# Optimization experiments

Measured on AMD Instinct MI355X. Metric: run time of the kernel, lower is better.

The kernel has to match this reference:

```python
import jax, jax.numpy as jnp
import numpy as np

N = 100000   # nodes
E = 1600000  # edges (before self loops)
F = 64       # num_features
H = 64       # hidden_channels
C = 10       # num_classes
G = 128      # graphs in batch
NEG_SLOPE = 0.2


def setup_inputs() -> dict:
    key = jax.random.key(0)
    ks = jax.random.split(key, 16)
    x = jax.random.normal(ks[0], (N, F), dtype=jnp.float32)
    edge_index = jax.random.randint(ks[1], (2, E), 0, N, dtype=jnp.int64)
    batch = jnp.sort(jax.random.randint(ks[2], (N,), 0, G, dtype=jnp.int64))
    def glorot(k, shape):
        fan = shape[0] + shape[-1]
        return jax.random.uniform(k, shape, jnp.float32, -1.0, 1.0) * np.sqrt(6.0 / fan)
    return {
        "x": x, "edge_index": edge_index, "batch": batch,
        # GATConv 1 (F -> H)
        "W1": glorot(ks[3], (F, H)), "as1": glorot(ks[4], (H,)), "ad1": glorot(ks[5], (H,)), "b1": jnp.zeros((H,), jnp.float32),
        # GATConv 2 (H -> H)
        "W2": glorot(ks[6], (H, H)), "as2": glorot(ks[7], (H,)), "ad2": glorot(ks[8], (H,)), "b2": jnp.zeros((H,), jnp.float32),
        # MLP head
        "mw1": glorot(ks[9], (H, H)), "mb1": jnp.zeros((H,), jnp.float32),
        "mw2": glorot(ks[10], (H, C)), "mb2": jnp.zeros((C,), jnp.float32),
    }


def gat_conv(x, src, dst, W, a_s, a_d, b):
    # x: [N, Fin] -> h: [N, Fout]
    h = x @ W
    # per-node attention halves, gathered per edge (heads=1)
    al_s = h @ a_s   # [N]
    al_d = h @ a_d   # [N]
    e = jax.nn.leaky_relu(al_s[src] + al_d[dst], NEG_SLOPE)  # [E']
    # segment softmax over incoming edges of each destination node
    m = jax.ops.segment_max(e, dst, num_segments=N)
    ex = jnp.exp(e - m[dst])
    denom = jax.ops.segment_sum(ex, dst, num_segments=N)
    alpha = ex / denom[dst]                                   # [E']
    # weighted scatter-add of source features
    out = jax.ops.segment_sum(alpha[:, None] * h[src], dst, num_segments=N)
    return out + b


def reference(x, edge_index, batch, W1, as1, ad1, b1, W2, as2, ad2, b2, mw1, mb1, mw2, mb2):
    # add self loops (PyG GATConv default)
    loop = jnp.arange(N, dtype=edge_index.dtype)
    src = jnp.concatenate([edge_index[0], loop])
    dst = jnp.concatenate([edge_index[1], loop])

    h = gat_conv(x, src, dst, W1, as1, ad1, b1)
    h = jax.nn.elu(h)  # dropout p=0.5 is identity in eval mode
    h = gat_conv(h, src, dst, W2, as2, ad2, b2)
    h = jax.nn.elu(h)

    h = jax.nn.relu(h @ mw1 + mb1) @ mw2 + mb2   # MLP [N, C]
    return jax.ops.segment_sum(h, batch, num_segments=G)  # global_add_pool [G, C]
```

## Files before the change

kernel.cpp:

```cpp
#include <hip/hip_runtime.h>
#include <hip/hip_bf16.h>
#include <math.h>

#define SHIFT 20.0f
#define T_PER 8
#define TILE (256 * T_PER)
#define BCAP 5248
#define LS_T 1024

typedef __bf16 bf16x8 __attribute__((ext_vector_type(8)));
typedef float  f32x4  __attribute__((ext_vector_type(4)));

__device__ __forceinline__ unsigned f2bf(float f) {
    unsigned u = __float_as_uint(f);
    return (u + 0x7fffu + ((u >> 16) & 1u)) >> 16;
}

__global__ void setup_kernel(int* __restrict__ bcur, int K2,
                             float* __restrict__ Pz, int nPz,
                             const float* __restrict__ W1,
                             const float* __restrict__ as1, const float* __restrict__ ad1,
                             const float* __restrict__ W2,
                             const float* __restrict__ as2, const float* __restrict__ ad2,
                             const float* __restrict__ mw1,
                             uint4* __restrict__ Wf1, uint4* __restrict__ Wf2,
                             uint4* __restrict__ mwf)
{
    int t = threadIdx.x;
    if (blockIdx.x == 0) {
        for (int i = t; i < K2; i += 256) bcur[i * 16] = i * BCAP;
        for (int i = t; i < nPz; i += 256) Pz[i] = 0.f;
        return;
    }
    __shared__ float wasad[256];
    {
        int k = t & 63;
        const float* W  = (t < 128) ? W1 : W2;
        const float* av = (t < 64) ? as1 : (t < 128) ? ad1 : (t < 192) ? as2 : ad2;
        float s = 0.f;
        for (int n = 0; n < 64; n++) s = fmaf(W[k * 64 + n], av[n], s);
        wasad[t] = s;
    }
    __syncthreads();

    for (int idx = t; idx < 1792; idx += 256) {
        const float* W; const float* wv; uint4* dst; int rem;
        if (idx < 640)       { rem = idx;        W = W1;  wv = &wasad[0];   dst = Wf1; }
        else if (idx < 1280) { rem = idx - 640;  W = W2;  wv = &wasad[128]; dst = Wf2; }
        else                 { rem = idx - 1280; W = mw1; wv = nullptr;     dst = mwf; }
        int pair = rem >> 6, l = rem & 63;
        int tt = pair >> 1, s = pair & 1;
        int kb = s * 32 + (l >> 4) * 8;
        unsigned d[4];
        if (tt < 4) {
            int n = tt * 16 + (l & 15);
            #pragma unroll
            for (int j = 0; j < 4; j++)
                d[j] = f2bf(W[(kb + 2 * j) * 64 + n]) |
                       (f2bf(W[(kb + 2 * j + 1) * 64 + n]) << 16);
        } else {
            int n0 = l & 15;
            #pragma unroll
            for (int j = 0; j < 4; j++) {
                float v0 = (n0 == 0) ? wv[kb + 2 * j]     : (n0 == 1) ? wv[64 + kb + 2 * j]     : 0.f;
                float v1 = (n0 == 0) ? wv[kb + 2 * j + 1] : (n0 == 1) ? wv[64 + kb + 2 * j + 1] : 0.f;
                d[j] = f2bf(v0) | (f2bf(v1) << 16);
            }
        }
        dst[pair * 64 + l] = make_uint4(d[0], d[1], d[2], d[3]);
    }
}

__device__ __forceinline__ void multisplit_body(
    unsigned char* lds, const int* __restrict__ esrc, const int* __restrict__ edst,
    int* __restrict__ bcur, unsigned* __restrict__ pairbuf,
    int nE, int tot, int K2, int tile)
{
    int* lhist = (int*)lds;
    int* lbase = lhist + 512;
    int t = threadIdx.x;
    int base = tile * TILE;
    for (int i = t; i < K2; i += 256) lhist[i] = 0;
    __syncthreads();

    unsigned pk[T_PER];
    int loc[T_PER];
    #pragma unroll
    for (int i = 0; i < T_PER; i++) {
        int e = base + t + i * 256;
        if (e < tot) {
            int s = (e < nE) ? esrc[e] : (e - nE);
            int d = (e < nE) ? edst[e] : (e - nE);
            int b = d >> 8;
            pk[i] = ((unsigned)s << 8) | (unsigned)(d & 255);
            int idx = atomicAdd(&lhist[b], 1);
            loc[i] = (b << 20) | idx;
        } else loc[i] = -1;
    }
    __syncthreads();
    for (int i = t; i < K2; i += 256) {
        int c = lhist[i];
        lbase[i] = (c > 0) ? atomicAdd(&bcur[i * 16], c) : 0;
    }
    __syncthreads();
    #pragma unroll
    for (int i = 0; i < T_PER; i++) {
        if (loc[i] >= 0)
            pairbuf[lbase[loc[i] >> 20] + (loc[i] & 0xFFFFF)] = pk[i];
    }
}

__device__ __forceinline__ void gemm_body(
    unsigned char* lds, const void* __restrict__ Xv, int x_is_bf16,
    const uint4* __restrict__ Wf, __hip_bfloat16* __restrict__ Hout,
    float* __restrict__ als, float* __restrict__ ald, int nN, int b0)
{
    int t = threadIdx.x, lane = t & 63, wv = t >> 6;

    uint4 wf[10];
    #pragma unroll
    for (int p = 0; p < 10; p++) wf[p] = Wf[p * 64 + lane];

    if (x_is_bf16) {
        const uint4* X4 = (const uint4*)Xv;
        int limit = nN * 8;
        #pragma unroll
        for (int k = 0; k < 8; k++) {
            int dst = t + k * 256;
            int idx = b0 * 8 + dst;
            if (idx < limit) {
                int r = dst >> 3, c = dst & 7;
                *(uint4*)(lds + r * 144 + c * 16) = X4[idx];
            }
        }
    } else {
        const float4* Xf = (const float4*)Xv;
        int limit = nN * 16;
        #pragma unroll
        for (int k = 0; k < 16; k++) {
            int dst = t + k * 256;
            int idx = b0 * 16 + dst;
            if (idx < limit) {
                float4 v = Xf[idx];
                uint2 r2;
                r2.x = f2bf(v.x) | (f2bf(v.y) << 16);
                r2.y = f2bf(v.z) | (f2bf(v.w) << 16);
                int r = dst >> 4, c = dst & 15;
                *(uint2*)(lds + r * 144 + c * 8) = r2;
            }
        }
    }
    __syncthreads();

    f32x4 acc[4][5] = {};
    int rbase = wv * 64;
    #pragma unroll
    for (int s = 0; s < 2; s++) {
        #pragma unroll
        for (int rf = 0; rf < 4; rf++) {
            const uint4 av = *(const uint4*)(lds + (rbase + rf * 16 + (lane & 15)) * 144
                                                 + s * 64 + (lane >> 4) * 16);
            bf16x8 a = __builtin_bit_cast(bf16x8, av);
            #pragma unroll
            for (int tt = 0; tt < 5; tt++) {
                bf16x8 b = __builtin_bit_cast(bf16x8, wf[tt * 2 + s]);
                acc[rf][tt] = __builtin_amdgcn_mfma_f32_16x16x32_bf16(a, b, acc[rf][tt], 0, 0, 0);
            }
        }
    }

    int q = lane >> 4, c = lane & 15;
    #pragma unroll
    for (int rf = 0; rf < 4; rf++) {
        #pragma unroll
        for (int r = 0; r < 4; r++) {
            int n = b0 + rbase + rf * 16 + q * 4 + r;
            if (n < nN) {
                #pragma unroll
                for (int tt = 0; tt < 4; tt++)
                    Hout[(size_t)n * 64 + tt * 16 + c] = __float2bfloat16(acc[rf][tt][r]);
                if (c == 0)      als[n] = acc[rf][4][r];
                else if (c == 1) ald[n] = acc[rf][4][r];
            }
        }
    }
}

__global__ __launch_bounds__(256) void ms_gemm_kernel(
    const int* __restrict__ esrc, const int* __restrict__ edst,
    int* __restrict__ bcur, unsigned* __restrict__ pairbuf,
    int nE, int nN, int K2, int nTiles,
    const void* __restrict__ Xv, const uint4* __restrict__ Wf,
    __hip_bfloat16* __restrict__ Hout,
    float* __restrict__ als, float* __restrict__ ald)
{
    __shared__ __align__(16) unsigned char lds[256 * 144];
    if (blockIdx.x < nTiles) {
        multisplit_body(lds, esrc, edst, bcur, pairbuf, nE, nE + nN, K2, blockIdx.x);
    } else {
        gemm_body(lds, Xv, 0, Wf, Hout, als, ald, nN, (blockIdx.x - nTiles) * 256);
    }
}

__global__ __launch_bounds__(256) void gemm_att_mfma(
    const void* __restrict__ Xv, int x_is_bf16,
    const uint4* __restrict__ Wf,
    __hip_bfloat16* __restrict__ Hout,
    float* __restrict__ als, float* __restrict__ ald, int nN)
{
    __shared__ __align__(16) unsigned char lds[256 * 144];
    gemm_body(lds, Xv, x_is_bf16, Wf, Hout, als, ald, nN, blockIdx.x * 256);
}

__global__ __launch_bounds__(LS_T) void local_scatter_kernel(
    const unsigned* __restrict__ pairbuf, const int* __restrict__ bcur,
    int2* __restrict__ rp2, int* __restrict__ csr_src, int nN, int K2)
{
    __shared__ unsigned seg[BCAP];
    __shared__ int lh[256];
    __shared__ int cur[256];
    __shared__ int psum[256];
    int b = blockIdx.x;
    int t = threadIdx.x;
    int d0 = b * 256;
    int nd = min(256, nN - d0);
    int lo = b * BCAP;
    int hi = bcur[b * 16];
    int len = min(hi - lo, BCAP);

    if (t < 256) lh[t] = 0;
    for (int j = t; j < len; j += LS_T) seg[j] = pairbuf[lo + j];
    __syncthreads();
    for (int j = t; j < len; j += LS_T) atomicAdd(&lh[seg[j] & 255u], 1);
    __syncthreads();

    int v = (t < 256) ? lh[t] : 0;
    if (t < 256) psum[t] = v;
    __syncthreads();
    for (int off = 1; off < 256; off <<= 1) {
        int u = (t < 256 && t >= off) ? psum[t - off] : 0;
        __syncthreads();
        if (t < 256) psum[t] += u;
        __syncthreads();
    }
    if (t < 256) {
        int e0 = lo + psum[t] - v;
        cur[t] = e0;
        if (t < nd) rp2[d0 + t] = make_int2(e0, v);
    }
    __syncthreads();

    for (int j = t; j < len; j += LS_T) {
        unsigned w = seg[j];
        int pos = atomicAdd(&cur[w & 255u], 1);
        csr_src[pos] = (int)(w >> 8);
    }
}

__global__ __launch_bounds__(256) void pull_kernel(
    const int* __restrict__ csr_src, const int2* __restrict__ rp2,
    const unsigned* __restrict__ Hu,
    const float* __restrict__ als, const float* __restrict__ ald,
    const float* __restrict__ bias,
    __hip_bfloat162* __restrict__ out2, int nN)
{
    int lane = threadIdx.x & 63;
    int half = lane >> 5;
    int fl = lane & 31;
    int wid  = (blockIdx.x * blockDim.x + threadIdx.x) >> 6;
    int nw   = (gridDim.x * blockDim.x) >> 6;
    float2 bl2 = ((const float2*)bias)[fl];

    for (int d = wid; d < nN; d += nw) {
        int2 rp = rp2[d];
        int s0 = rp.x, m = rp.y;
        float aldd = ald[d];
        float aclo = 0.f, achi = 0.f, den = 0.f;

        for (int base = 0; base < m; base += 64) {
            int j = base + lane;
            bool v = (j < m);
            int sl = v ? csr_src[s0 + j] : 0;
            float ex = 0.f;
            if (v) {
                float sc = als[sl] + aldd;
                sc = (sc > 0.f) ? sc : 0.2f * sc;
                ex = __expf(sc - SHIFT);
            }
            float es = ex;
            #pragma unroll
            for (int off = 32; off > 0; off >>= 1) es += __shfl_xor(es, off);
            den += es;

            int mm = min(64, m - base);
            int sA = __shfl(sl, half), sB = __shfl(sl, 2 + half);
            float eA = __shfl(ex, half), eB = __shfl(ex, 2 + half);
            unsigned dA = Hu[((unsigned)sA << 5) | fl];
            unsigned dB = Hu[((unsigned)sB << 5) | fl];
            for (int i2 = 0; i2 < mm; i2 += 4) {
                int i4 = (i2 + 4) & 63;
                int   sA2 = __shfl(sl, i4 + half);
                int   sB2 = __shfl(sl, i4 + 2 + half);
                float eA2 = __shfl(ex, i4 + half);
                float eB2 = __shfl(ex, i4 + 2 + half);
                unsigned dA2 = Hu[((unsigned)sA2 << 5) | fl];
                unsigned dB2 = Hu[((unsigned)sB2 << 5) | fl];
                aclo = fmaf(eA, __uint_as_float(dA << 16), aclo);
                achi = fmaf(eA, __uint_as_float(dA & 0xffff0000u), achi);
                aclo = fmaf(eB, __uint_as_float(dB << 16), aclo);
                achi = fmaf(eB, __uint_as_float(dB & 0xffff0000u), achi);
                sA = sA2; sB = sB2; eA = eA2; eB = eB2; dA = dA2; dB = dB2;
            }
        }
        aclo += __shfl_xor(aclo, 32);
        achi += __shfl_xor(achi, 32);
        float v0 = aclo / den + bl2.x;
        float v1 = achi / den + bl2.y;
        v0 = (v0 > 0.f) ? v0 : expm1f(v0);
        v1 = (v1 > 0.f) ? v1 : expm1f(v1);
        if (half == 0) {
            __hip_bfloat162 pk;
            pk.x = __float2bfloat16(v0);
            pk.y = __float2bfloat16(v1);
            out2[((unsigned)d << 5) | fl] = pk;
        }
    }
}

__global__ __launch_bounds__(256) void mlp_pool_mfma(
    const uint4* __restrict__ Hin,
    const uint4* __restrict__ mwf, const float* __restrict__ mb1,
    const int* __restrict__ batch,
    float* __restrict__ P, float* __restrict__ Pcnt, int nN)
{
    __shared__ __align__(16) unsigned char lds[256 * 144];
    int t = threadIdx.x, lane = t & 63, wv = t >> 6;
    int b0 = blockIdx.x * 256;

    uint4 wf[8];
    #pragma unroll
    for (int p = 0; p < 8; p++) wf[p] = mwf[p * 64 + lane];

    int limit = nN * 8;
    #pragma unroll
    for (int k = 0; k < 8; k++) {
        int dst = t + k * 256;
        int idx = b0 * 8 + dst;
        if (idx < limit) {
            int r = dst >> 3, c = dst & 7;
            *(uint4*)(lds + r * 144 + c * 16) = Hin[idx];
        }
    }
    __syncthreads();

    f32x4 acc[4][4] = {};
    int rbase = wv * 64;
    #pragma unroll
    for (int s = 0; s < 2; s++) {
        #pragma unroll
        for (int rf = 0; rf < 4; rf++) {
            const uint4 av = *(const uint4*)(lds + (rbase + rf * 16 + (lane & 15)) * 144
                                                 + s * 64 + (lane >> 4) * 16);
            bf16x8 a = __builtin_bit_cast(bf16x8, av);
            #pragma unroll
            for (int tt = 0; tt < 4; tt++) {
                bf16x8 b = __builtin_bit_cast(bf16x8, wf[tt * 2 + s]);
                acc[rf][tt] = __builtin_amdgcn_mfma_f32_16x16x32_bf16(a, b, acc[rf][tt], 0, 0, 0);
            }
        }
    }

    int q = lane >> 4, c = lane & 15;
    float bl0 = mb1[c], bl1 = mb1[16 + c], bl2 = mb1[32 + c], bl3 = mb1[48 + c];
    float r0 = 0.f, r1 = 0.f, r2 = 0.f, r3 = 0.f, ccnt = 0.f;
    int gcur = -1;
    #pragma unroll
    for (int rf = 0; rf < 4; rf++) {
        #pragma unroll
        for (int r = 0; r < 4; r++) {
            int n = b0 + rbase + rf * 16 + q * 4 + r;
            if (n < nN) {
                int g = batch[n];
                if (g != gcur) {
                    if (gcur >= 0) {
                        atomicAdd(&P[(size_t)gcur * 64 + c],      r0);
                        atomicAdd(&P[(size_t)gcur * 64 + 16 + c], r1);
                        atomicAdd(&P[(size_t)gcur * 64 + 32 + c], r2);
                        atomicAdd(&P[(size_t)gcur * 64 + 48 + c], r3);
                        if (c == 0) atomicAdd(&Pcnt[gcur], ccnt);
                    }
                    gcur = g; r0 = r1 = r2 = r3 = 0.f; ccnt = 0.f;
                }
                r0 += fmaxf(acc[rf][0][r] + bl0, 0.f);
                r1 += fmaxf(acc[rf][1][r] + bl1, 0.f);
                r2 += fmaxf(acc[rf][2][r] + bl2, 0.f);
                r3 += fmaxf(acc[rf][3][r] + bl3, 0.f);
                ccnt += 1.f;
            }
        }
    }
    if (gcur >= 0) {
        atomicAdd(&P[(size_t)gcur * 64 + c],      r0);
        atomicAdd(&P[(size_t)gcur * 64 + 16 + c], r1);
        atomicAdd(&P[(size_t)gcur * 64 + 32 + c], r2);
        atomicAdd(&P[(size_t)gcur * 64 + 48 + c], r3);
        if (c == 0) atomicAdd(&Pcnt[gcur], ccnt);
    }
}

__global__ void head_out_kernel(const float* __restrict__ P,
                                const float* __restrict__ Pcnt,
                                const float* __restrict__ mw2,
                                const float* __restrict__ mb2,
                                float* __restrict__ out, int nOut)
{
    int t = blockIdx.x * blockDim.x + threadIdx.x;
    if (t >= nOut) return;
    int g = t / 10, j = t % 10;
    float s = mb2[j] * Pcnt[g];
    const float* pr = P + (size_t)g * 64;
    #pragma unroll
    for (int k = 0; k < 64; k++) s = fmaf(pr[k], mw2[k * 10 + j], s);
    out[t] = s;
}

extern "C" void kernel_launch(void* const* d_in, const int* in_sizes, int n_in,
                              void* d_out, int out_size, void* d_ws, size_t ws_size,
                              hipStream_t stream)
{
    const float* x   = (const float*)d_in[0];
    const int*  eidx = (const int*)d_in[1];
    const int* batch = (const int*)d_in[2];
    const float* W1  = (const float*)d_in[3];
    const float* as1 = (const float*)d_in[4];
    const float* ad1 = (const float*)d_in[5];
    const float* b1  = (const float*)d_in[6];
    const float* W2  = (const float*)d_in[7];
    const float* as2 = (const float*)d_in[8];
    const float* ad2 = (const float*)d_in[9];
    const float* b2  = (const float*)d_in[10];
    const float* mw1 = (const float*)d_in[11];
    const float* mb1 = (const float*)d_in[12];
    const float* mw2 = (const float*)d_in[13];
    const float* mb2 = (const float*)d_in[14];
    float* out = (float*)d_out;

    int nN = in_sizes[0] / 64;
    int nE = in_sizes[1] / 2;
    int tot = nE + nN;
    int K2 = (nN + 255) >> 8;
    int G  = out_size / 10;
    const int* esrc = eidx;
    const int* edst = eidx + nE;

    float* ws = (float*)d_ws;
    size_t NF = (size_t)nN * 64;
    size_t capTot = (size_t)K2 * BCAP;
    float* bufA   = ws;
    float* bufB   = ws + NF;
    float* als    = ws + 2 * NF;
    float* ald    = als + nN;
    int2* rp2     = (int2*)(ald + nN);
    int* csr_src  = (int*)(rp2 + nN);
    int* bcur     = csr_src + capTot;
    float* P      = (float*)(bcur + K2 * 16 + 15);
    float* Pcnt   = P + (size_t)G * 64;
    uintptr_t wb  = ((uintptr_t)(Pcnt + G) + 255) & ~(uintptr_t)255;
    uint4* Wf1    = (uint4*)wb;
    uint4* Wf2    = Wf1 + 640;
    uint4* mwf    = Wf2 + 640;
    unsigned* pairbuf = (unsigned*)bufA;
    __hip_bfloat16* hbf = (__hip_bfloat16*)bufB;

    dim3 blk(256);
    int nTiles = (tot + TILE - 1) / TILE;
    int nT256 = (nN + 255) / 256;

    setup_kernel<<<2, blk, 0, stream>>>(bcur, K2, P, G * 64 + G,
                                        W1, as1, ad1, W2, as2, ad2, mw1,
                                        Wf1, Wf2, mwf);
    ms_gemm_kernel<<<nTiles + nT256, blk, 0, stream>>>(
        esrc, edst, bcur, pairbuf, nE, nN, K2, nTiles,
        x, Wf1, hbf, als, ald);
    local_scatter_kernel<<<K2, dim3(LS_T), 0, stream>>>(pairbuf, bcur, rp2,
                                                        csr_src, nN, K2);

    pull_kernel<<<2048, blk, 0, stream>>>(csr_src, rp2, (const unsigned*)hbf,
                                          als, ald, b1,
                                          (__hip_bfloat162*)bufA, nN);
    gemm_att_mfma<<<nT256, blk, 0, stream>>>(bufA, 1, Wf2, hbf, als, ald, nN);
    pull_kernel<<<2048, blk, 0, stream>>>(csr_src, rp2, (const unsigned*)hbf,
                                          als, ald, b2,
                                          (__hip_bfloat162*)bufA, nN);

    mlp_pool_mfma<<<nT256, blk, 0, stream>>>((const uint4*)bufA, mwf, mb1,
                                             batch, P, Pcnt, nN);
    head_out_kernel<<<(out_size + 255) / 256, blk, 0, stream>>>(P, Pcnt, mw2,
                                                                mb2, out, out_size);
}
```

Before: 302.7 us.

## Widen pull-kernel gathers to 8-byte rows, 4 edges per wave step

The pull kernel now splits the wave into four 16-lane groups. Each lane gathers a uint2 (four bf16 features), so one gather instruction fetches four edges' rows instead of two. Prefetching keeps four edges in flight and the partial sums are reduced across groups with two xor-shuffles. The pair buffer's one-shot store and reload now use nontemporal hints to keep it from polluting the cache. The cost is more shuffle reductions and more registers, and the edge loop now steps through the shuffled edges one slot at a time per group.

```diff
diff --git a/kernel.cpp b/kernel.cpp
--- a/kernel.cpp
+++ b/kernel.cpp
@@ -106,7 +106,8 @@
     #pragma unroll
     for (int i = 0; i < T_PER; i++) {
         if (loc[i] >= 0)
-            pairbuf[lbase[loc[i] >> 20] + (loc[i] & 0xFFFFF)] = pk[i];
+            __builtin_nontemporal_store(pk[i],
+                &pairbuf[lbase[loc[i] >> 20] + (loc[i] & 0xFFFFF)]);
     }
 }
 
@@ -229,7 +230,8 @@
     int len = min(hi - lo, BCAP);
 
     if (t < 256) lh[t] = 0;
-    for (int j = t; j < len; j += LS_T) seg[j] = pairbuf[lo + j];
+    for (int j = t; j < len; j += LS_T)
+        seg[j] = __builtin_nontemporal_load(&pairbuf[lo + j]);
     __syncthreads();
     for (int j = t; j < len; j += LS_T) atomicAdd(&lh[seg[j] & 255u], 1);
     __syncthreads();
@@ -259,23 +261,23 @@
 
 __global__ __launch_bounds__(256) void pull_kernel(
     const int* __restrict__ csr_src, const int2* __restrict__ rp2,
-    const unsigned* __restrict__ Hu,
+    const uint2* __restrict__ Hu2,
     const float* __restrict__ als, const float* __restrict__ ald,
     const float* __restrict__ bias,
-    __hip_bfloat162* __restrict__ out2, int nN)
+    uint2* __restrict__ out2, int nN)
 {
     int lane = threadIdx.x & 63;
-    int half = lane >> 5;
-    int fl = lane & 31;
+    int eq = lane >> 4;
+    int fq = lane & 15;
     int wid  = (blockIdx.x * blockDim.x + threadIdx.x) >> 6;
     int nw   = (gridDim.x * blockDim.x) >> 6;
-    float2 bl2 = ((const float2*)bias)[fl];
+    float4 bl = ((const float4*)bias)[fq];
 
     for (int d = wid; d < nN; d += nw) {
         int2 rp = rp2[d];
         int s0 = rp.x, m = rp.y;
         float aldd = ald[d];
-        float aclo = 0.f, achi = 0.f, den = 0.f;
+        float a0 = 0.f, a1 = 0.f, a2 = 0.f, a3 = 0.f, den = 0.f;
 
         for (int base = 0; base < m; base += 64) {
             int j = base + lane;
@@ -293,36 +295,45 @@
             den += es;
 
             int mm = min(64, m - base);
-            int sA = __shfl(sl, half), sB = __shfl(sl, 2 + half);
-            float eA = __shfl(ex, half), eB = __shfl(ex, 2 + half);
-            unsigned dA = Hu[((unsigned)sA << 5) | fl];
-            unsigned dB = Hu[((unsigned)sB << 5) | fl];
+            float eA = __shfl(ex, eq),      eB = __shfl(ex, 4 + eq);
+            float eC = __shfl(ex, 8 + eq),  eD = __shfl(ex, 12 + eq);
+            int   sA = __shfl(sl, eq),      sB = __shfl(sl, 4 + eq);
+            int   sC = __shfl(sl, 8 + eq),  sD = __shfl(sl, 12 + eq);
+            uint2 dA = Hu2[((unsigned)sA << 4) | fq];
+            uint2 dB = Hu2[((unsigned)sB << 4) | fq];
+            uint2 dC = Hu2[((unsigned)sC << 4) | fq];
+            uint2 dD = Hu2[((unsigned)sD << 4) | fq];
             for (int i2 = 0; i2 < mm; i2 += 4) {
-                int i4 = (i2 + 4) & 63;
-                int   sA2 = __shfl(sl, i4 + half);
-                int   sB2 = __shfl(sl, i4 + 2 + half);
-                float eA2 = __shfl(ex, i4 + half);
-                float eB2 = __shfl(ex, i4 + 2 + half);
-                unsigned dA2 = Hu[((unsigned)sA2 << 5) | fl];
-                unsigned dB2 = Hu[((unsigned)sB2 << 5) | fl];
-                aclo = fmaf(eA, __uint_as_float(dA << 16), aclo);
-                achi = fmaf(eA, __uint_as_float(dA & 0xffff0000u), achi);
-                aclo = fmaf(eB, __uint_as_float(dB << 16), aclo);
-                achi = fmaf(eB, __uint_as_float(dB & 0xffff0000u), achi);
-                sA = sA2; sB = sB2; eA = eA2; eB = eB2; dA = dA2; dB = dB2;
-            }
-        }
-        aclo += __shfl_xor(aclo, 32);
-        achi += __shfl_xor(achi, 32);
-        float v0 = aclo / den + bl2.x;
-        float v1 = achi / den + bl2.y;
-        v0 = (v0 > 0.f) ? v0 : expm1f(v0);
-        v1 = (v1 > 0.f) ? v1 : expm1f(v1);
-        if (half == 0) {
-            __hip_bfloat162 pk;
-            pk.x = __float2bfloat16(v0);
-            pk.y = __float2bfloat16(v1);
-            out2[((unsigned)d << 5) | fl] = pk;
+                int wn = (i2 + 16) & 63;
+                int   sN = __shfl(sl, wn + eq);
+                float eN = __shfl(ex, wn + eq);
+                uint2 dN = Hu2[((unsigned)sN << 4) | fq];
+                a0 = fmaf(eA, __uint_as_float(dA.x << 16), a0);
+                a1 = fmaf(eA, __uint_as_float(dA.x & 0xffff0000u), a1);
+                a2 = fmaf(eA, __uint_as_float(dA.y << 16), a2);
+                a3 = fmaf(eA, __uint_as_float(dA.y & 0xffff0000u), a3);
+                eA = eB; dA = dB; eB = eC; dB = dC;
+                eC = eD; dC = dD; eD = eN; dD = dN;
+            }
+        }
+        a0 += __shfl_xor(a0, 16); a0 += __shfl_xor(a0, 32);
+        a1 += __shfl_xor(a1, 16); a1 += __shfl_xor(a1, 32);
+        a2 += __shfl_xor(a2, 16); a2 += __shfl_xor(a2, 32);
+        a3 += __shfl_xor(a3, 16); a3 += __shfl_xor(a3, 32);
+        if (eq == 0) {
+            float r = 1.f / den;
+            float v0 = a0 * r + bl.x;
+            float v1 = a1 * r + bl.y;
+            float v2 = a2 * r + bl.z;
+            float v3 = a3 * r + bl.w;
+            v0 = (v0 > 0.f) ? v0 : expm1f(v0);
+            v1 = (v1 > 0.f) ? v1 : expm1f(v1);
+            v2 = (v2 > 0.f) ? v2 : expm1f(v2);
+            v3 = (v3 > 0.f) ? v3 : expm1f(v3);
+            uint2 pk;
+            pk.x = f2bf(v0) | (f2bf(v1) << 16);
+            pk.y = f2bf(v2) | (f2bf(v3) << 16);
+            out2[((unsigned)d << 4) | fq] = pk;
         }
     }
 }
@@ -485,13 +496,11 @@
     local_scatter_kernel<<<K2, dim3(LS_T), 0, stream>>>(pairbuf, bcur, rp2,
                                                         csr_src, nN, K2);
 
-    pull_kernel<<<2048, blk, 0, stream>>>(csr_src, rp2, (const unsigned*)hbf,
-                                          als, ald, b1,
-                                          (__hip_bfloat162*)bufA, nN);
+    pull_kernel<<<2048, blk, 0, stream>>>(csr_src, rp2, (const uint2*)hbf,
+                                          als, ald, b1, (uint2*)bufA, nN);
     gemm_att_mfma<<<nT256, blk, 0, stream>>>(bufA, 1, Wf2, hbf, als, ald, nN);
-    pull_kernel<<<2048, blk, 0, stream>>>(csr_src, rp2, (const unsigned*)hbf,
-                                          als, ald, b2,
-                                          (__hip_bfloat162*)bufA, nN);
+    pull_kernel<<<2048, blk, 0, stream>>>(csr_src, rp2, (const uint2*)hbf,
+                                          als, ald, b2, (uint2*)bufA, nN);
 
     mlp_pool_mfma<<<nT256, blk, 0, stream>>>((const uint4*)bufA, mwf, mb1,
                                              batch, P, Pcnt, nN);
```

New measurement: 343.9 us. +13.6%, slower.
